# Performance work log

Hardware: AMD Instinct MI355X
Metric: run time of the kernel (lower is better)

## Reference

```python
import jax, jax.numpy as jnp
import numpy as np

D, DFF, H, NLAYERS, B, L, U = 1536, 2048, 8, 2, 16, 64, 64
EPS = 1e-5


def _ln(x, w, b):
    mu = jnp.mean(x, axis=-1, keepdims=True)
    var = jnp.mean((x - mu) ** 2, axis=-1, keepdims=True)
    return (x - mu) / jnp.sqrt(var + EPS) * w + b


def _mha(q_in, kv_in, qkv_w, qkv_b, out_w, out_b, mask):
    # torch nn.MultiheadAttention: packed in_proj [3D,D], out_proj [D,D]
    d = q_in.shape[-1]
    hd = d // H
    wq, wk, wv = jnp.split(qkv_w, 3, axis=0)
    bq, bk, bv = jnp.split(qkv_b, 3, axis=0)
    q = q_in @ wq.T + bq
    k = kv_in @ wk.T + bk
    v = kv_in @ wv.T + bv
    def heads(t):
        b_, s_, _ = t.shape
        return t.reshape(b_, s_, H, hd).transpose(0, 2, 1, 3)  # [B,H,S,hd]
    q, k, v = heads(q), heads(k), heads(v)
    scores = jnp.einsum('bhqd,bhkd->bhqk', q, k) / jnp.sqrt(jnp.float32(hd))
    if mask is not None:
        scores = scores + mask  # [Sq,Sk] broadcast
    attn = jax.nn.softmax(scores, axis=-1)
    o = jnp.einsum('bhqk,bhkd->bhqd', attn, v)
    b_, _, s_, _ = o.shape
    o = o.transpose(0, 2, 1, 3).reshape(b_, s_, d)
    return o @ out_w.T + out_b


def setup_inputs() -> dict:
    key = jax.random.key(0)
    ks = jax.random.split(key, 16)
    f = lambda k, shp: (jax.random.normal(k, shp, jnp.float32) * 0.02)
    Lyr = NLAYERS
    return {
        'x': jax.random.normal(ks[0], (B, L, U, D), jnp.float32),
        'pooler_w': f(ks[1], (1, D)),
        'pooler_b': jnp.zeros((1,), jnp.float32),
        'pos_embed': f(ks[2], (1, 128, D)),
        'sa_qkv_w': f(ks[3], (Lyr, 3 * D, D)),
        'sa_qkv_b': jnp.zeros((Lyr, 3 * D), jnp.float32),
        'sa_out_w': f(ks[4], (Lyr, D, D)),
        'sa_out_b': jnp.zeros((Lyr, D), jnp.float32),
        'ca_qkv_w': f(ks[5], (Lyr, 3 * D, D)),
        'ca_qkv_b': jnp.zeros((Lyr, 3 * D), jnp.float32),
        'ca_out_w': f(ks[6], (Lyr, D, D)),
        'ca_out_b': jnp.zeros((Lyr, D), jnp.float32),
        'ff1_w': f(ks[7], (Lyr, DFF, D)),
        'ff1_b': jnp.zeros((Lyr, DFF), jnp.float32),
        'ff2_w': f(ks[8], (Lyr, D, DFF)),
        'ff2_b': jnp.zeros((Lyr, D), jnp.float32),
        'ln1_w': jnp.ones((Lyr, D), jnp.float32),
        'ln1_b': jnp.zeros((Lyr, D), jnp.float32),
        'ln2_w': jnp.ones((Lyr, D), jnp.float32),
        'ln2_b': jnp.zeros((Lyr, D), jnp.float32),
        'ln3_w': jnp.ones((Lyr, D), jnp.float32),
        'ln3_b': jnp.zeros((Lyr, D), jnp.float32),
    }


def reference(x, pooler_w, pooler_b, pos_embed,
              sa_qkv_w, sa_qkv_b, sa_out_w, sa_out_b,
              ca_qkv_w, ca_qkv_b, ca_out_w, ca_out_b,
              ff1_w, ff1_b, ff2_w, ff2_b,
              ln1_w, ln1_b, ln2_w, ln2_b, ln3_w, ln3_b):
    b, l, u, d = x.shape
    # SelfAttentionPooling over utterance tokens (vectorized over dialogue dim)
    logits = jnp.einsum('blud,d->blu', x, pooler_w[0]) + pooler_b[0]
    att = jax.nn.softmax(logits, axis=-1)
    pooled = jnp.einsum('blu,blud->bld', att, x)

    pos = pos_embed[:, :l, :]
    memory = pooled + pos
    tgt = pooled + pos
    causal = jnp.triu(jnp.full((l, l), -jnp.inf, jnp.float32), 1)

    h = tgt
    for i in range(NLAYERS):
        # post-norm TransformerDecoderLayer (torch default norm_first=False)
        h = _ln(h + _mha(h, h, sa_qkv_w[i], sa_qkv_b[i], sa_out_w[i], sa_out_b[i], causal),
                ln1_w[i], ln1_b[i])
        h = _ln(h + _mha(h, memory, ca_qkv_w[i], ca_qkv_b[i], ca_out_w[i], ca_out_b[i], None),
                ln2_w[i], ln2_b[i])
        ff = jax.nn.relu(h @ ff1_w[i].T + ff1_b[i]) @ ff2_w[i].T + ff2_b[i]
        h = _ln(h + ff, ln3_w[i], ln3_b[i])

    # loop over prefixes t=1..L-1 taking the last position == causal positions 0..L-2
    return h[:, : l - 1, :]
```

## Files before the change

kernel.cpp:

```cpp
#include <hip/hip_runtime.h>
#include <math.h>

#define D_MODEL 1536
#define NH      8
#define HD      192
#define BB      16
#define LL      64
#define UU      64
#define NTOK    1024
#define EPSF    1e-5f

typedef __bf16 bf16;
typedef __bf16 bf16x4_t __attribute__((ext_vector_type(4)));
typedef __bf16 bf16x8_t __attribute__((ext_vector_type(8)));
typedef float  f32x4_t  __attribute__((ext_vector_type(4)));

__device__ __forceinline__ void gload_lds16(const bf16* g, bf16* l) {
    __builtin_amdgcn_global_load_lds((const __attribute__((address_space(1))) void*)g,
                                     (__attribute__((address_space(3))) void*)l, 16, 0, 0);
}

__global__ __launch_bounds__(256)
void cvt_kernel(const float* __restrict__ s, bf16* __restrict__ d, int n4)
{
    int i = blockIdx.x * 256 + threadIdx.x;
    const int stride = gridDim.x * 256;
    for (; i < n4; i += stride) {
        const float4 v = ((const float4*)s)[i];
        bf16x4_t o = { (bf16)v.x, (bf16)v.y, (bf16)v.z, (bf16)v.w };
        ((bf16x4_t*)d)[i] = o;
    }
}

__global__ __launch_bounds__(256)
void fusedpool_kernel(const float* __restrict__ x, const float* __restrict__ pw,
                      const float* __restrict__ pb, const float* __restrict__ pos,
                      float* __restrict__ h, bf16* __restrict__ hb,
                      bf16* __restrict__ memb)
{
    __shared__ float red[2][4];
    const int t = threadIdx.x, wave = t >> 6, lane = t & 63;
    const int bl = blockIdx.x, l = bl & (LL - 1);
    const float* xb = x + (size_t)bl * UU * D_MODEL;

    float pwr[6];
#pragma unroll
    for (int j = 0; j < 6; ++j) pwr[j] = pw[t + j * 256];
    const float pb0 = pb[0];

    float xv[2][6];
#pragma unroll
    for (int j = 0; j < 6; ++j) xv[0][j] = xb[t + j * 256];

    float m = -__builtin_inff(), den = 0.f;
    float acc[6] = {0.f, 0.f, 0.f, 0.f, 0.f, 0.f};

    for (int u = 0; u < UU; ++u) {
        const int cur = u & 1;
        if (u < UU - 1) {
            const float* xn = xb + (size_t)(u + 1) * D_MODEL;
#pragma unroll
            for (int j = 0; j < 6; ++j) xv[cur ^ 1][j] = xn[t + j * 256];
        }
        float p = 0.f;
#pragma unroll
        for (int j = 0; j < 6; ++j) p += xv[cur][j] * pwr[j];
#pragma unroll
        for (int off = 32; off; off >>= 1) p += __shfl_xor(p, off, 64);
        if (lane == 0) red[cur][wave] = p;
        __syncthreads();
        const float logit = red[cur][0] + red[cur][1] + red[cur][2] + red[cur][3] + pb0;
        const float nm = fmaxf(m, logit);
        const float sc = __expf(m - nm);
        const float w  = __expf(logit - nm);
#pragma unroll
        for (int j = 0; j < 6; ++j) acc[j] = acc[j] * sc + w * xv[cur][j];
        den = den * sc + w;
        m = nm;
    }

    const float inv = 1.f / den;
    const size_t db = (size_t)bl * D_MODEL;
    const int pp = l * D_MODEL;
#pragma unroll
    for (int j = 0; j < 6; ++j) {
        const int d = t + j * 256;
        const float v = acc[j] * inv + pos[pp + d];
        h[db + d] = v;
        hb[db + d] = (bf16)v;
        memb[db + d] = (bf16)v;
    }
}

#define GBM 64
#define GBN 128

template<int MODE>
__global__ __launch_bounds__(256, 3)
void gemm_bf16_kernel(const bf16* __restrict__ A, const bf16* __restrict__ W,
                      const float* __restrict__ bias, float* __restrict__ C,
                      bf16* __restrict__ Cb, int N, int K)
{
    __shared__ bf16 As[2][GBM * 64];
    __shared__ bf16 Bs[2][GBN * 64];
    const int t = threadIdx.x, wave = t >> 6, lane = t & 63;

    const int T = gridDim.x;
    const int fid = blockIdx.x;
    const int vid = (fid & 7) * (T >> 3) + (fid >> 3);
    const int m0 = (vid & 15) * GBM;
    const int n0 = (vid >> 4) * GBN;

    const int wr = wave >> 1, wc = wave & 1;
    const int frow = lane & 15, kq = lane >> 4, s = frow & 7;
    const int lr = lane >> 3;
    const int g8 = ((lane & 7) ^ lr) * 8;

    f32x4_t acc[2][4] = {};

    const bf16* Abase = A + (size_t)(m0 + wave * 8 + lr) * K + g8;
    const bf16* Wbase = W + (size_t)(n0 + wave * 8 + lr) * K + g8;

#pragma unroll
    for (int i = 0; i < 2; ++i)
        gload_lds16(Abase + (size_t)(i * 32) * K, &As[0][wave * 512] + i * 2048);
#pragma unroll
    for (int i = 0; i < 4; ++i)
        gload_lds16(Wbase + (size_t)(i * 32) * K, &Bs[0][wave * 512] + i * 2048);
    __syncthreads();

    const int nt = K >> 6;
    int cur = 0;
    for (int tt = 0; tt < nt; ++tt) {
        if (tt + 1 < nt) {
            const int k0 = (tt + 1) << 6;
#pragma unroll
            for (int i = 0; i < 2; ++i)
                gload_lds16(Abase + k0 + (size_t)(i * 32) * K, &As[cur ^ 1][wave * 512] + i * 2048);
#pragma unroll
            for (int i = 0; i < 4; ++i)
                gload_lds16(Wbase + k0 + (size_t)(i * 32) * K, &Bs[cur ^ 1][wave * 512] + i * 2048);
        }
#pragma unroll
        for (int kk = 0; kk < 2; ++kk) {
            const int gg = (((kk << 2) | kq) ^ s) * 8;
            bf16x8_t af[2], bv[4];
#pragma unroll
            for (int mi = 0; mi < 2; ++mi)
                af[mi] = *(const bf16x8_t*)&As[cur][(wr * 32 + mi * 16 + frow) * 64 + gg];
#pragma unroll
            for (int ni = 0; ni < 4; ++ni)
                bv[ni] = *(const bf16x8_t*)&Bs[cur][(wc * 64 + ni * 16 + frow) * 64 + gg];
#pragma unroll
            for (int mi = 0; mi < 2; ++mi)
#pragma unroll
                for (int ni = 0; ni < 4; ++ni)
                    acc[mi][ni] = __builtin_amdgcn_mfma_f32_16x16x32_bf16(af[mi], bv[ni], acc[mi][ni], 0, 0, 0);
        }
        __syncthreads();
        cur ^= 1;
    }

    const int crow = m0 + wr * 32 + kq * 4;
    const int ccol = n0 + wc * 64 + frow;
#pragma unroll
    for (int mi = 0; mi < 2; ++mi)
#pragma unroll
        for (int ni = 0; ni < 4; ++ni) {
            const int col = ccol + ni * 16;
            const float bvv = bias[col];
            const int rb = crow + mi * 16;
#pragma unroll
            for (int j = 0; j < 4; ++j) {
                float v = acc[mi][ni][j] + bvv;
                if (MODE == 0) {
                    C[(size_t)(rb + j) * N + col] = v;
                } else {
                    Cb[(size_t)(rb + j) * N + col] = (bf16)fmaxf(v, 0.f);
                }
            }
        }
}

template<bool CAUSAL>
__global__ __launch_bounds__(256)
void attn_kernel(const float* __restrict__ qbuf, int qstride, int qoff0,
                 const float* __restrict__ kbuf, int kstride, int koff0,
                 const float* __restrict__ vbuf, int vstride, int voff0,
                 bf16* __restrict__ out)
{
    __shared__ float kv[HD * 64];
    __shared__ float sc[16 * 64];
    const int t = threadIdx.x, wave = t >> 6, lane = t & 63;
    const int bh = blockIdx.x >> 2, qh = blockIdx.x & 3;
    const int b = bh >> 3, hh = bh & 7;
    const int t0 = b * 64;
    const float scale = rsqrtf((float)HD);

    for (int i = 0; i < 48; ++i) {
        const int idx = t + i * 256;
        const int r = idx / HD, c = idx % HD;
        kv[c * 64 + (r ^ (c & 31))] = kbuf[(size_t)(t0 + r) * kstride + koff0 + hh * HD + c];
    }
    __syncthreads();

    for (int qi = 0; qi < 4; ++qi) {
        const int ql = wave * 4 + qi;
        const int q = qh * 16 + ql;
        const float* qr = qbuf + (size_t)(t0 + q) * qstride + qoff0 + hh * HD;
        float a = 0.f;
#pragma unroll 8
        for (int d = 0; d < HD; ++d)
            a += qr[d] * kv[d * 64 + (lane ^ (d & 31))];
        a *= scale;
        if (CAUSAL && lane > q) a = -__builtin_inff();
        float m = a;
#pragma unroll
        for (int off = 32; off; off >>= 1) m = fmaxf(m, __shfl_xor(m, off, 64));
        float e = (CAUSAL && lane > q) ? 0.f : __expf(a - m);
        float s = e;
#pragma unroll
        for (int off = 32; off; off >>= 1) s += __shfl_xor(s, off, 64);
        sc[ql * 64 + lane] = e / s;
    }
    __syncthreads();

    for (int i = 0; i < 48; ++i) {
        const int idx = t + i * 256;
        const int r = idx / HD, c = idx % HD;
        kv[r * HD + c] = vbuf[(size_t)(t0 + r) * vstride + voff0 + hh * HD + c];
    }
    __syncthreads();

    for (int qi = 0; qi < 4; ++qi) {
        const int ql = wave * 4 + qi;
        const int q = qh * 16 + ql;
        float o0 = 0.f, o1 = 0.f, o2 = 0.f;
#pragma unroll 8
        for (int k = 0; k < 64; ++k) {
            const float p = sc[ql * 64 + k];
            o0 += p * kv[k * HD + lane];
            o1 += p * kv[k * HD + 64 + lane];
            o2 += p * kv[k * HD + 128 + lane];
        }
        bf16* op = out + (size_t)(t0 + q) * D_MODEL + hh * HD;
        op[lane] = (bf16)o0; op[64 + lane] = (bf16)o1; op[128 + lane] = (bf16)o2;
    }
}

__global__ __launch_bounds__(256)
void ln_kernel(const float* __restrict__ a, const float* __restrict__ r,
               const float* __restrict__ w, const float* __restrict__ bb,
               float* __restrict__ out, bf16* __restrict__ outb)
{
    __shared__ float red[8];
    const int tok = blockIdx.x, t = threadIdx.x;
    const int wave = t >> 6, lane = t & 63;
    const float* ap = a + (size_t)tok * D_MODEL;
    const float* rp = r + (size_t)tok * D_MODEL;
    float v[6];
    float s = 0.f;
#pragma unroll
    for (int j = 0; j < 6; ++j) { v[j] = ap[t + j * 256] + rp[t + j * 256]; s += v[j]; }
#pragma unroll
    for (int off = 32; off; off >>= 1) s += __shfl_xor(s, off, 64);
    if (lane == 0) red[wave] = s;
    __syncthreads();
    const float mu = (red[0] + red[1] + red[2] + red[3]) * (1.f / D_MODEL);
    float s2 = 0.f;
#pragma unroll
    for (int j = 0; j < 6; ++j) { const float d = v[j] - mu; s2 += d * d; }
#pragma unroll
    for (int off = 32; off; off >>= 1) s2 += __shfl_xor(s2, off, 64);
    if (lane == 0) red[4 + wave] = s2;
    __syncthreads();
    const float var = (red[4] + red[5] + red[6] + red[7]) * (1.f / D_MODEL);
    const float inv = rsqrtf(var + EPSF);
#pragma unroll
    for (int j = 0; j < 6; ++j) {
        const int d = t + j * 256;
        const float o = (v[j] - mu) * inv * w[d] + bb[d];
        out[(size_t)tok * D_MODEL + d] = o;
        outb[(size_t)tok * D_MODEL + d] = (bf16)o;
    }
}

__global__ __launch_bounds__(256)
void slice_kernel(const float* __restrict__ h, float* __restrict__ out)
{
    const int i = blockIdx.x * 256 + threadIdx.x;
    if (i >= BB * 63 * (D_MODEL / 4)) return;
    const int d4 = i % (D_MODEL / 4);
    const int tl = i / (D_MODEL / 4);
    const int b = tl / 63, l = tl % 63;
    ((float4*)out)[i] = ((const float4*)(h + (size_t)(b * 64 + l) * D_MODEL))[d4];
}

extern "C" void kernel_launch(void* const* d_in, const int* in_sizes, int n_in,
                              void* d_out, int out_size, void* d_ws, size_t ws_size,
                              hipStream_t stream)
{
    (void)in_sizes; (void)n_in; (void)out_size; (void)ws_size;
    const float* x        = (const float*)d_in[0];
    const float* pooler_w = (const float*)d_in[1];
    const float* pooler_b = (const float*)d_in[2];
    const float* pos      = (const float*)d_in[3];
    const float* sa_qkv_w = (const float*)d_in[4];
    const float* sa_qkv_b = (const float*)d_in[5];
    const float* sa_out_w = (const float*)d_in[6];
    const float* sa_out_b = (const float*)d_in[7];
    const float* ca_qkv_w = (const float*)d_in[8];
    const float* ca_qkv_b = (const float*)d_in[9];
    const float* ca_out_w = (const float*)d_in[10];
    const float* ca_out_b = (const float*)d_in[11];
    const float* ff1_w    = (const float*)d_in[12];
    const float* ff1_b    = (const float*)d_in[13];
    const float* ff2_w    = (const float*)d_in[14];
    const float* ff2_b    = (const float*)d_in[15];
    const float* ln1_w    = (const float*)d_in[16];
    const float* ln1_b    = (const float*)d_in[17];
    const float* ln2_w    = (const float*)d_in[18];
    const float* ln2_b    = (const float*)d_in[19];
    const float* ln3_w    = (const float*)d_in[20];
    const float* ln3_b    = (const float*)d_in[21];
    float* outp = (float*)d_out;

    char* ws = (char*)d_ws;
    size_t off = 0;
    auto alloc = [&](size_t bytes) { char* p = ws + off; off += (bytes + 255) & ~(size_t)255; return p; };

    const size_t E_QKV = (size_t)4608 * D_MODEL;
    const size_t E_SQ  = (size_t)D_MODEL * D_MODEL;
    const size_t E_F1  = (size_t)2048 * D_MODEL;

    bf16* wb_sa_qkv = (bf16*)alloc(2 * E_QKV * 2);
    bf16* wb_sa_out = (bf16*)alloc(2 * E_SQ * 2);
    bf16* wb_ca_qkv = (bf16*)alloc(2 * E_QKV * 2);
    bf16* wb_ca_out = (bf16*)alloc(2 * E_SQ * 2);
    bf16* wb_ff1    = (bf16*)alloc(2 * E_F1 * 2);
    bf16* wb_ff2    = (bf16*)alloc(2 * E_F1 * 2);
    float* h     = (float*)alloc((size_t)NTOK * D_MODEL * 4);
    bf16*  hb    = (bf16*) alloc((size_t)NTOK * D_MODEL * 2);
    bf16*  memb  = (bf16*) alloc((size_t)NTOK * D_MODEL * 2);
    float* qkv   = (float*)alloc((size_t)NTOK * 4608 * 4);
    bf16*  attno = (bf16*) alloc((size_t)NTOK * D_MODEL * 2);
    float* proj  = (float*)alloc((size_t)NTOK * D_MODEL * 4);
    bf16*  ffmid = (bf16*) alloc((size_t)NTOK * 2048 * 2);

    float* cq  = qkv;
    float* ckv = qkv + (size_t)NTOK * D_MODEL;

    cvt_kernel<<<1024, 256, 0, stream>>>(sa_qkv_w, wb_sa_qkv, (int)(2 * E_QKV / 4));
    cvt_kernel<<<512,  256, 0, stream>>>(sa_out_w, wb_sa_out, (int)(2 * E_SQ  / 4));
    cvt_kernel<<<1024, 256, 0, stream>>>(ca_qkv_w, wb_ca_qkv, (int)(2 * E_QKV / 4));
    cvt_kernel<<<512,  256, 0, stream>>>(ca_out_w, wb_ca_out, (int)(2 * E_SQ  / 4));
    cvt_kernel<<<512,  256, 0, stream>>>(ff1_w,    wb_ff1,    (int)(2 * E_F1  / 4));
    cvt_kernel<<<512,  256, 0, stream>>>(ff2_w,    wb_ff2,    (int)(2 * E_F1  / 4));

    fusedpool_kernel<<<NTOK, 256, 0, stream>>>(x, pooler_w, pooler_b, pos, h, hb, memb);

    for (int i = 0; i < 2; ++i) {
        gemm_bf16_kernel<0><<<16 * 36, 256, 0, stream>>>(
            hb, wb_sa_qkv + (size_t)i * E_QKV, sa_qkv_b + (size_t)i * 4608,
            qkv, nullptr, 4608, D_MODEL);
        attn_kernel<true><<<BB * NH * 4, 256, 0, stream>>>(
            qkv, 4608, 0, qkv, 4608, 1536, qkv, 4608, 3072, attno);
        gemm_bf16_kernel<0><<<16 * 12, 256, 0, stream>>>(
            attno, wb_sa_out + (size_t)i * E_SQ, sa_out_b + (size_t)i * D_MODEL,
            proj, nullptr, D_MODEL, D_MODEL);
        ln_kernel<<<NTOK, 256, 0, stream>>>(h, proj, ln1_w + i * D_MODEL, ln1_b + i * D_MODEL, h, hb);

        gemm_bf16_kernel<0><<<16 * 12, 256, 0, stream>>>(
            hb, wb_ca_qkv + (size_t)i * E_QKV, ca_qkv_b + (size_t)i * 4608,
            cq, nullptr, D_MODEL, D_MODEL);
        gemm_bf16_kernel<0><<<16 * 24, 256, 0, stream>>>(
            memb, wb_ca_qkv + (size_t)i * E_QKV + (size_t)1536 * D_MODEL,
            ca_qkv_b + (size_t)i * 4608 + 1536,
            ckv, nullptr, 3072, D_MODEL);
        attn_kernel<false><<<BB * NH * 4, 256, 0, stream>>>(
            cq, 1536, 0, ckv, 3072, 0, ckv, 3072, 1536, attno);
        gemm_bf16_kernel<0><<<16 * 12, 256, 0, stream>>>(
            attno, wb_ca_out + (size_t)i * E_SQ, ca_out_b + (size_t)i * D_MODEL,
            proj, nullptr, D_MODEL, D_MODEL);
        ln_kernel<<<NTOK, 256, 0, stream>>>(h, proj, ln2_w + i * D_MODEL, ln2_b + i * D_MODEL, h, hb);

        gemm_bf16_kernel<1><<<16 * 16, 256, 0, stream>>>(
            hb, wb_ff1 + (size_t)i * E_F1, ff1_b + (size_t)i * 2048,
            nullptr, ffmid, 2048, D_MODEL);
        gemm_bf16_kernel<0><<<16 * 12, 256, 0, stream>>>(
            ffmid, wb_ff2 + (size_t)i * E_F1, ff2_b + (size_t)i * D_MODEL,
            proj, nullptr, D_MODEL, 2048);
        ln_kernel<<<NTOK, 256, 0, stream>>>(h, proj, ln3_w + i * D_MODEL, ln3_b + i * D_MODEL, h, hb);
    }

    slice_kernel<<<(BB * 63 * (D_MODEL / 4) + 255) / 256, 256, 0, stream>>>(h, outp);
}
```

Measured before the change: 826.7 us.

## Use 8-wave GEMM blocks, batch cross-attn KV projections, merge weight conversion

The GEMM kernel now runs 512 threads (8 waves) per 64x128 tile, so each wave computes a 32x32 sub-tile instead of 32x64. This is meant to raise latency hiding and MFMA issue parallelism for these small-M GEMMs. The cross-attention K/V projections of both layers depend only on memory, so they are hoisted out of the layer loop into one dual GEMM launch, which gives a larger grid but needs extra buffers. The six weight-conversion kernels are merged into one launch. The main risk is that halving per-wave work adds barrier and LDS overhead per MFMA.

```diff
diff --git a/kernel.cpp b/kernel.cpp
--- a/kernel.cpp
+++ b/kernel.cpp
@@ -21,14 +21,24 @@
 }
 
 __global__ __launch_bounds__(256)
-void cvt_kernel(const float* __restrict__ s, bf16* __restrict__ d, int n4)
-{
-    int i = blockIdx.x * 256 + threadIdx.x;
-    const int stride = gridDim.x * 256;
-    for (; i < n4; i += stride) {
-        const float4 v = ((const float4*)s)[i];
+void cvt_all_kernel(const float* __restrict__ s0, const float* __restrict__ s1,
+                    const float* __restrict__ s2, const float* __restrict__ s3,
+                    const float* __restrict__ s4, const float* __restrict__ s5,
+                    bf16* __restrict__ dst)
+{
+    const int c0 = 3538944, c1 = 4718592, c2 = 8257536,
+              c3 = 9437184, c4 = 11010048, c5 = 12582912;
+    for (int i = blockIdx.x * 256 + threadIdx.x; i < c5; i += gridDim.x * 256) {
+        const float* s; int j;
+        if      (i < c0) { s = s0; j = i; }
+        else if (i < c1) { s = s1; j = i - c0; }
+        else if (i < c2) { s = s2; j = i - c1; }
+        else if (i < c3) { s = s3; j = i - c2; }
+        else if (i < c4) { s = s4; j = i - c3; }
+        else             { s = s5; j = i - c4; }
+        const float4 v = ((const float4*)s)[j];
         bf16x4_t o = { (bf16)v.x, (bf16)v.y, (bf16)v.z, (bf16)v.w };
-        ((bf16x4_t*)d)[i] = o;
+        ((bf16x4_t*)dst)[i] = o;
     }
 }
 
@@ -92,41 +102,39 @@
     }
 }
 
-#define GBM 64
-#define GBN 128
-
-template<int MODE>
-__global__ __launch_bounds__(256, 3)
-void gemm_bf16_kernel(const bf16* __restrict__ A, const bf16* __restrict__ W,
-                      const float* __restrict__ bias, float* __restrict__ C,
-                      bf16* __restrict__ Cb, int N, int K)
-{
-    __shared__ bf16 As[2][GBM * 64];
-    __shared__ bf16 Bs[2][GBN * 64];
+template<int MODE, bool DUAL>
+__global__ __launch_bounds__(512, 4)
+void gemm8_kernel(const bf16* __restrict__ A, const bf16* __restrict__ W,
+                  const float* __restrict__ bias, void* __restrict__ Cv,
+                  int N, int K, int split,
+                  const bf16* __restrict__ A2, const bf16* __restrict__ W2,
+                  const float* __restrict__ bias2, void* __restrict__ Cv2, int N2)
+{
+    __shared__ bf16 As[2][64 * 64];
+    __shared__ bf16 Bs[2][128 * 64];
     const int t = threadIdx.x, wave = t >> 6, lane = t & 63;
 
-    const int T = gridDim.x;
-    const int fid = blockIdx.x;
-    const int vid = (fid & 7) * (T >> 3) + (fid >> 3);
-    const int m0 = (vid & 15) * GBM;
-    const int n0 = (vid >> 4) * GBN;
-
-    const int wr = wave >> 1, wc = wave & 1;
+    const int T = gridDim.x, fid = blockIdx.x;
+    int vid = (fid & 7) * (T >> 3) + (fid >> 3);
+    const bf16* Ap = A; const bf16* Wp = W; const float* bp = bias;
+    void* Cp = Cv; int Nn = N;
+    if (DUAL && vid >= split) { vid -= split; Ap = A2; Wp = W2; bp = bias2; Cp = Cv2; Nn = N2; }
+    const int m0 = (vid & 15) * 64;
+    const int n0 = (vid >> 4) * 128;
+
+    const int wm = wave >> 2, wn = wave & 3;
     const int frow = lane & 15, kq = lane >> 4, s = frow & 7;
     const int lr = lane >> 3;
     const int g8 = ((lane & 7) ^ lr) * 8;
 
-    f32x4_t acc[2][4] = {};
-
-    const bf16* Abase = A + (size_t)(m0 + wave * 8 + lr) * K + g8;
-    const bf16* Wbase = W + (size_t)(n0 + wave * 8 + lr) * K + g8;
-
-#pragma unroll
-    for (int i = 0; i < 2; ++i)
-        gload_lds16(Abase + (size_t)(i * 32) * K, &As[0][wave * 512] + i * 2048);
-#pragma unroll
-    for (int i = 0; i < 4; ++i)
-        gload_lds16(Wbase + (size_t)(i * 32) * K, &Bs[0][wave * 512] + i * 2048);
+    f32x4_t acc[2][2] = {};
+
+    const bf16* Abase = Ap + (size_t)(m0 + wave * 8 + lr) * K + g8;
+    const bf16* Wbase = Wp + (size_t)(n0 + wave * 8 + lr) * K + g8;
+
+    gload_lds16(Abase, &As[0][wave * 512]);
+    gload_lds16(Wbase, &Bs[0][wave * 512]);
+    gload_lds16(Wbase + (size_t)64 * K, &Bs[0][4096 + wave * 512]);
     __syncthreads();
 
     const int nt = K >> 6;
@@ -134,49 +142,46 @@
     for (int tt = 0; tt < nt; ++tt) {
         if (tt + 1 < nt) {
             const int k0 = (tt + 1) << 6;
-#pragma unroll
-            for (int i = 0; i < 2; ++i)
-                gload_lds16(Abase + k0 + (size_t)(i * 32) * K, &As[cur ^ 1][wave * 512] + i * 2048);
-#pragma unroll
-            for (int i = 0; i < 4; ++i)
-                gload_lds16(Wbase + k0 + (size_t)(i * 32) * K, &Bs[cur ^ 1][wave * 512] + i * 2048);
+            gload_lds16(Abase + k0, &As[cur ^ 1][wave * 512]);
+            gload_lds16(Wbase + k0, &Bs[cur ^ 1][wave * 512]);
+            gload_lds16(Wbase + k0 + (size_t)64 * K, &Bs[cur ^ 1][4096 + wave * 512]);
         }
 #pragma unroll
         for (int kk = 0; kk < 2; ++kk) {
             const int gg = (((kk << 2) | kq) ^ s) * 8;
-            bf16x8_t af[2], bv[4];
+            bf16x8_t af[2], bv[2];
 #pragma unroll
             for (int mi = 0; mi < 2; ++mi)
-                af[mi] = *(const bf16x8_t*)&As[cur][(wr * 32 + mi * 16 + frow) * 64 + gg];
-#pragma unroll
-            for (int ni = 0; ni < 4; ++ni)
-                bv[ni] = *(const bf16x8_t*)&Bs[cur][(wc * 64 + ni * 16 + frow) * 64 + gg];
+                af[mi] = *(const bf16x8_t*)&As[cur][(wm * 32 + mi * 16 + frow) * 64 + gg];
+#pragma unroll
+            for (int ni = 0; ni < 2; ++ni)
+                bv[ni] = *(const bf16x8_t*)&Bs[cur][(wn * 32 + ni * 16 + frow) * 64 + gg];
 #pragma unroll
             for (int mi = 0; mi < 2; ++mi)
 #pragma unroll
-                for (int ni = 0; ni < 4; ++ni)
+                for (int ni = 0; ni < 2; ++ni)
                     acc[mi][ni] = __builtin_amdgcn_mfma_f32_16x16x32_bf16(af[mi], bv[ni], acc[mi][ni], 0, 0, 0);
         }
         __syncthreads();
         cur ^= 1;
     }
 
-    const int crow = m0 + wr * 32 + kq * 4;
-    const int ccol = n0 + wc * 64 + frow;
+    const int crow = m0 + wm * 32 + kq * 4;
+    const int ccol = n0 + wn * 32 + frow;
 #pragma unroll
     for (int mi = 0; mi < 2; ++mi)
 #pragma unroll
-        for (int ni = 0; ni < 4; ++ni) {
+        for (int ni = 0; ni < 2; ++ni) {
             const int col = ccol + ni * 16;
-            const float bvv = bias[col];
+            const float bvv = bp[col];
             const int rb = crow + mi * 16;
 #pragma unroll
             for (int j = 0; j < 4; ++j) {
                 float v = acc[mi][ni][j] + bvv;
                 if (MODE == 0) {
-                    C[(size_t)(rb + j) * N + col] = v;
+                    ((float*)Cp)[(size_t)(rb + j) * Nn + col] = v;
                 } else {
-                    Cb[(size_t)(rb + j) * N + col] = (bf16)fmaxf(v, 0.f);
+                    ((bf16*)Cp)[(size_t)(rb + j) * Nn + col] = (bf16)fmaxf(v, 0.f);
                 }
             }
         }
@@ -343,53 +348,52 @@
     bf16*  hb    = (bf16*) alloc((size_t)NTOK * D_MODEL * 2);
     bf16*  memb  = (bf16*) alloc((size_t)NTOK * D_MODEL * 2);
     float* qkv   = (float*)alloc((size_t)NTOK * 4608 * 4);
+    float* cq    = (float*)alloc((size_t)NTOK * D_MODEL * 4);
+    float* ckv0  = (float*)alloc((size_t)NTOK * 3072 * 4);
+    float* ckv1  = (float*)alloc((size_t)NTOK * 3072 * 4);
     bf16*  attno = (bf16*) alloc((size_t)NTOK * D_MODEL * 2);
     float* proj  = (float*)alloc((size_t)NTOK * D_MODEL * 4);
     bf16*  ffmid = (bf16*) alloc((size_t)NTOK * 2048 * 2);
 
-    float* cq  = qkv;
-    float* ckv = qkv + (size_t)NTOK * D_MODEL;
-
-    cvt_kernel<<<1024, 256, 0, stream>>>(sa_qkv_w, wb_sa_qkv, (int)(2 * E_QKV / 4));
-    cvt_kernel<<<512,  256, 0, stream>>>(sa_out_w, wb_sa_out, (int)(2 * E_SQ  / 4));
-    cvt_kernel<<<1024, 256, 0, stream>>>(ca_qkv_w, wb_ca_qkv, (int)(2 * E_QKV / 4));
-    cvt_kernel<<<512,  256, 0, stream>>>(ca_out_w, wb_ca_out, (int)(2 * E_SQ  / 4));
-    cvt_kernel<<<512,  256, 0, stream>>>(ff1_w,    wb_ff1,    (int)(2 * E_F1  / 4));
-    cvt_kernel<<<512,  256, 0, stream>>>(ff2_w,    wb_ff2,    (int)(2 * E_F1  / 4));
-
+    cvt_all_kernel<<<2048, 256, 0, stream>>>(sa_qkv_w, sa_out_w, ca_qkv_w,
+                                             ca_out_w, ff1_w, ff2_w, wb_sa_qkv);
     fusedpool_kernel<<<NTOK, 256, 0, stream>>>(x, pooler_w, pooler_b, pos, h, hb, memb);
 
+    gemm8_kernel<0, true><<<768, 512, 0, stream>>>(
+        memb, wb_ca_qkv + (size_t)1536 * D_MODEL, ca_qkv_b + 1536,
+        ckv0, 3072, D_MODEL, 384,
+        memb, wb_ca_qkv + E_QKV + (size_t)1536 * D_MODEL, ca_qkv_b + 4608 + 1536,
+        ckv1, 3072);
+
     for (int i = 0; i < 2; ++i) {
-        gemm_bf16_kernel<0><<<16 * 36, 256, 0, stream>>>(
+        float* ckv = i ? ckv1 : ckv0;
+
+        gemm8_kernel<0, false><<<16 * 36, 512, 0, stream>>>(
             hb, wb_sa_qkv + (size_t)i * E_QKV, sa_qkv_b + (size_t)i * 4608,
-            qkv, nullptr, 4608, D_MODEL);
+            qkv, 4608, D_MODEL, 0, nullptr, nullptr, nullptr, nullptr, 0);
         attn_kernel<true><<<BB * NH * 4, 256, 0, stream>>>(
             qkv, 4608, 0, qkv, 4608, 1536, qkv, 4608, 3072, attno);
-        gemm_bf16_kernel<0><<<16 * 12, 256, 0, stream>>>(
+        gemm8_kernel<0, false><<<16 * 12, 512, 0, stream>>>(
             attno, wb_sa_out + (size_t)i * E_SQ, sa_out_b + (size_t)i * D_MODEL,
-            proj, nullptr, D_MODEL, D_MODEL);
+            proj, D_MODEL, D_MODEL, 0, nullptr, nullptr, nullptr, nullptr, 0);
         ln_kernel<<<NTOK, 256, 0, stream>>>(h, proj, ln1_w + i * D_MODEL, ln1_b + i * D_MODEL, h, hb);
 
-        gemm_bf16_kernel<0><<<16 * 12, 256, 0, stream>>>(
+        gemm8_kernel<0, false><<<16 * 12, 512, 0, stream>>>(
             hb, wb_ca_qkv + (size_t)i * E_QKV, ca_qkv_b + (size_t)i * 4608,
-            cq, nullptr, D_MODEL, D_MODEL);
-        gemm_bf16_kernel<0><<<16 * 24, 256, 0, stream>>>(
-            memb, wb_ca_qkv + (size_t)i * E_QKV + (size_t)1536 * D_MODEL,
-            ca_qkv_b + (size_t)i * 4608 + 1536,
-            ckv, nullptr, 3072, D_MODEL);
+            cq, D_MODEL, D_MODEL, 0, nullptr, nullptr, nullptr, nullptr, 0);
         attn_kernel<false><<<BB * NH * 4, 256, 0, stream>>>(
             cq, 1536, 0, ckv, 3072, 0, ckv, 3072, 1536, attno);
-        gemm_bf16_kernel<0><<<16 * 12, 256, 0, stream>>>(
+        gemm8_kernel<0, false><<<16 * 12, 512, 0, stream>>>(
             attno, wb_ca_out + (size_t)i * E_SQ, ca_out_b + (size_t)i * D_MODEL,
-            proj, nullptr, D_MODEL, D_MODEL);
+            proj, D_MODEL, D_MODEL, 0, nullptr, nullptr, nullptr, nullptr, 0);
         ln_kernel<<<NTOK, 256, 0, stream>>>(h, proj, ln2_w + i * D_MODEL, ln2_b + i * D_MODEL, h, hb);
 
-        gemm_bf16_kernel<1><<<16 * 16, 256, 0, stream>>>(
+        gemm8_kernel<1, false><<<16 * 16, 512, 0, stream>>>(
             hb, wb_ff1 + (size_t)i * E_F1, ff1_b + (size_t)i * 2048,
-            nullptr, ffmid, 2048, D_MODEL);
-        gemm_bf16_kernel<0><<<16 * 12, 256, 0, stream>>>(
+            ffmid, 2048, D_MODEL, 0, nullptr, nullptr, nullptr, nullptr, 0);
+        gemm8_kernel<0, false><<<16 * 12, 512, 0, stream>>>(
             ffmid, wb_ff2 + (size_t)i * E_F1, ff2_b + (size_t)i * D_MODEL,
-            proj, nullptr, D_MODEL, 2048);
+            proj, D_MODEL, 2048, 0, nullptr, nullptr, nullptr, nullptr, 0);
         ln_kernel<<<NTOK, 256, 0, stream>>>(h, proj, ln3_w + i * D_MODEL, ln3_b + i * D_MODEL, h, hb);
     }
 
```

New measurement: 773.8 us. -6.4%, faster.
